# Kernel optimization log

Measured on AMD Instinct MI355X. Metric: run time of the kernel, lower is better.

The kernel has to match this reference:

```python
import jax, jax.numpy as jnp
import numpy as np

VOCAB = 32000
EMBED_DIM = 256
NUM_RULES = 100
BATCH, SEQ = 4, 2048


def setup_inputs() -> dict:
    key = jax.random.key(0)
    k1, k2, k3, k4 = jax.random.split(key, 4)
    token_ids = jax.random.randint(k1, (BATCH, SEQ), 0, VOCAB)
    base_embeddings = jax.random.normal(k2, (VOCAB, EMBED_DIM), dtype=jnp.float32)
    rule_transform = jax.random.normal(k3, (NUM_RULES, EMBED_DIM, EMBED_DIM), dtype=jnp.float32)
    token_rules = jax.random.randint(k4, (VOCAB,), 0, NUM_RULES)
    return {
        "token_ids": token_ids,
        "base_embeddings": base_embeddings,
        "rule_transform": rule_transform,
        "token_rules": token_rules,
    }


def reference(token_ids, base_embeddings, rule_transform, token_rules):
    # base_embeds: [B, S, D]
    base_embeds = base_embeddings[token_ids]
    # per-token rule index: [B, S]
    rule_indices = token_rules[token_ids]
    # per-token (D, D) transform gathered from rule bank: [B, S, D, D]
    rule_matrices = rule_transform[rule_indices]
    # token-routed matvec: out[b,s,e] = sum_d base[b,s,d] * M[b,s,d,e]
    return jnp.einsum('bsd,bsde->bse', base_embeds, rule_matrices)
```

## Files before the change

kernel.cpp:

```cpp
#include <hip/hip_runtime.h>


#define NTOK   8192
#define NRULE  100
#define DIM    256
#define TCH    32
#define NSEG   32
#define SEGCAP 256
#define GSTR   64
#define NCONV  (NRULE * 8)
#define NBLK_A (NCONV + NSEG)

#define BFRAG_U16   (NRULE * 8 * 16 * 64 * 8)
#define WS_SEGCNT   (BFRAG_U16 / 2)
#define WS_SEGLIST  (WS_SEGCNT + NRULE * NSEG)
#define WS_TOTAL_INT (WS_SEGLIST + NRULE * NSEG * SEGCAP)
#define WS_BYTES    ((size_t)WS_TOTAL_INT * 4)

typedef __attribute__((ext_vector_type(8))) short bf16x8;
typedef __attribute__((ext_vector_type(4))) float f32x4;

__device__ __forceinline__ unsigned short f2bf(float f) {
    union { float f; unsigned int u; } c; c.f = f;
    unsigned int u = c.u;
    u = (u + 0x7FFFu + ((u >> 16) & 1u)) >> 16;
    return (unsigned short)u;
}

__global__ __launch_bounds__(256)
void conv_scatter_kernel(const int* __restrict__ token_ids,
                         const int* __restrict__ token_rules,
                         const float* __restrict__ M,
                         int* __restrict__ ws,
                         unsigned short* __restrict__ bf) {
    const int tid = threadIdx.x;
    const int bid = blockIdx.x;

    if (bid >= NCONV) {
        __shared__ int cur[NRULE];
        const int b = bid - NCONV;
        if (tid < NRULE) cur[tid] = 0;
        __syncthreads();
        const int tok = b * SEGCAP + tid;
        const int id  = token_ids[tok];
        const int r   = token_rules[id];
        const int slot = atomicAdd(&cur[r], 1);
        ws[WS_SEGLIST + (r * NSEG + b) * SEGCAP + slot] = tok;
        __syncthreads();
        if (tid < NRULE) ws[WS_SEGCNT + tid * NSEG + b] = cur[tid];
        return;
    }

    __shared__ unsigned short sb[32][DIM];
    const int r  = bid >> 3;
    const int ks = bid & 7;
    const float4* M4 = reinterpret_cast<const float4*>(M) + ((size_t)r * 256 + ks * 32) * 64;
    #pragma unroll
    for (int j = 0; j < 8; ++j) {
        int idx = j * 256 + tid;
        int kl = idx >> 6, c4 = idx & 63;
        float4 v = M4[kl * 64 + c4];
        sb[kl][c4 * 4 + 0] = f2bf(v.x);
        sb[kl][c4 * 4 + 1] = f2bf(v.y);
        sb[kl][c4 * 4 + 2] = f2bf(v.z);
        sb[kl][c4 * 4 + 3] = f2bf(v.w);
    }
    __syncthreads();

    uint4* outp = reinterpret_cast<uint4*>(bf) + ((size_t)(r * 8 + ks) * 16) * 64;
    #pragma unroll
    for (int it = 0; it < 4; ++it) {
        int w = it * 256 + tid;
        int ct = w >> 6, l = w & 63;
        int kb = (l >> 4) * 8, cc = ct * 16 + (l & 15);
        unsigned int d0 = sb[kb + 0][cc] | ((unsigned int)sb[kb + 1][cc] << 16);
        unsigned int d1 = sb[kb + 2][cc] | ((unsigned int)sb[kb + 3][cc] << 16);
        unsigned int d2 = sb[kb + 4][cc] | ((unsigned int)sb[kb + 5][cc] << 16);
        unsigned int d3 = sb[kb + 6][cc] | ((unsigned int)sb[kb + 7][cc] << 16);
        outp[ct * 64 + l] = make_uint4(d0, d1, d2, d3);
    }
}

__global__ __launch_bounds__(512)
void gemm_kernel(const int* __restrict__ token_ids,
                 const float* __restrict__ base_emb,
                 const int* __restrict__ ws,
                 const unsigned short* __restrict__ bfrag,
                 float* __restrict__ out) {
    const int xcd  = blockIdx.x & 7;
    const int base = blockIdx.x >> 3;
    const int tid  = threadIdx.x;
    const int wave = tid >> 6, lane = tid & 63;

    __shared__ unsigned short sa[8 * 2 * 64 * 8];
    __shared__ int sst[TCH];
    __shared__ int s_scnt[13][NSEG];
    __shared__ int s_soff[13][NSEG + 1];
    __shared__ int s_tot[13];
    __shared__ int s_choff[14];

    if (tid < 13 * NSEG) {
        int i = tid >> 5, b = tid & (NSEG - 1);
        int r = xcd + 8 * i;
        s_scnt[i][b] = (r < NRULE) ? ws[WS_SEGCNT + r * NSEG + b] : 0;
    }
    __syncthreads();
    if (tid < 13) {
        int acc = 0;
        #pragma unroll
        for (int b = 0; b < NSEG; ++b) { s_soff[tid][b] = acc; acc += s_scnt[tid][b]; }
        s_soff[tid][NSEG] = acc;
        s_tot[tid] = acc;
    }
    __syncthreads();
    if (tid == 0) {
        int acc = 0; s_choff[0] = 0;
        #pragma unroll
        for (int i = 0; i < 13; ++i) { acc += (s_tot[i] + TCH - 1) / TCH; s_choff[i + 1] = acc; }
    }
    __syncthreads();
    const int total_ch = s_choff[13];

    for (int slot = base; slot < total_ch; slot += GSTR) {
        int i = 0;
        #pragma unroll
        for (int k = 1; k < 13; ++k) if (slot >= s_choff[k]) i = k;
        const int r = xcd + 8 * i;
        const int j = slot - s_choff[i];

        __syncthreads();
        if (tid < TCH) {
            int idx = j * TCH + tid;
            int tok = -1;
            if (idx < s_tot[i]) {
                int lo = 0, hi = NSEG - 1;
                while (lo < hi) {
                    int mid = (lo + hi + 1) >> 1;
                    if (s_soff[i][mid] <= idx) lo = mid; else hi = mid - 1;
                }
                tok = ws[WS_SEGLIST + (r * NSEG + lo) * SEGCAP + (idx - s_soff[i][lo])];
            }
            sst[tid] = tok;
        }
        __syncthreads();

        {
            const int s = tid >> 4, q = tid & 15;
            const int pos = sst[s];
            const int tt = s >> 4, lr = s & 15;
            const float4* row4 = nullptr;
            if (pos >= 0)
                row4 = reinterpret_cast<const float4*>(base_emb + (size_t)token_ids[pos] * DIM);
            #pragma unroll
            for (int jj = 0; jj < 4; ++jj) {
                float4 v = row4 ? row4[q * 4 + jj] : make_float4(0.f, 0.f, 0.f, 0.f);
                const int k0 = q * 16 + jj * 4;
                const int ks = k0 >> 5, koff = k0 & 31;
                const int l = lr | ((koff >> 3) << 4);
                const int e0 = koff & 7;
                ushort4 p;
                p.x = f2bf(v.x); p.y = f2bf(v.y); p.z = f2bf(v.z); p.w = f2bf(v.w);
                *reinterpret_cast<ushort4*>(&sa[((ks * 2 + tt) * 64 + l) * 8 + e0]) = p;
            }
        }
        __syncthreads();

        f32x4 acc[2][2];
        #pragma unroll
        for (int tt = 0; tt < 2; ++tt)
            #pragma unroll
            for (int ctl = 0; ctl < 2; ++ctl)
                acc[tt][ctl] = (f32x4){0.f, 0.f, 0.f, 0.f};

        const bf16x8* Af = reinterpret_cast<const bf16x8*>(sa);
        const bf16x8* Bf = reinterpret_cast<const bf16x8*>(bfrag) + (size_t)r * 8 * 16 * 64;
        const int ct0 = wave * 2;

        #pragma unroll
        for (int ks = 0; ks < 8; ++ks) {
            const bf16x8 a0 = Af[(ks * 2 + 0) * 64 + lane];
            const bf16x8 a1 = Af[(ks * 2 + 1) * 64 + lane];
            const bf16x8 b0 = Bf[(ks * 16 + ct0 + 0) * 64 + lane];
            const bf16x8 b1 = Bf[(ks * 16 + ct0 + 1) * 64 + lane];
            acc[0][0] = __builtin_amdgcn_mfma_f32_16x16x32_bf16(a0, b0, acc[0][0], 0, 0, 0);
            acc[0][1] = __builtin_amdgcn_mfma_f32_16x16x32_bf16(a0, b1, acc[0][1], 0, 0, 0);
            acc[1][0] = __builtin_amdgcn_mfma_f32_16x16x32_bf16(a1, b0, acc[1][0], 0, 0, 0);
            acc[1][1] = __builtin_amdgcn_mfma_f32_16x16x32_bf16(a1, b1, acc[1][1], 0, 0, 0);
        }

        #pragma unroll
        for (int tt = 0; tt < 2; ++tt) {
            #pragma unroll
            for (int reg = 0; reg < 4; ++reg) {
                const int row = tt * 16 + (lane >> 4) * 4 + reg;
                const int pos = sst[row];
                if (pos >= 0) {
                    #pragma unroll
                    for (int ctl = 0; ctl < 2; ++ctl) {
                        const int col = (ct0 + ctl) * 16 + (lane & 15);
                        out[(size_t)pos * DIM + col] = acc[tt][ctl][reg];
                    }
                }
            }
        }
    }
}

__global__ __launch_bounds__(256, 4)
void rule_embed_fallback(const int* __restrict__ token_ids,
                         const float* __restrict__ base_emb,
                         const float* __restrict__ rule_mats,
                         const int* __restrict__ token_rules,
                         float* __restrict__ out, int n_tokens) {
    const int wave = threadIdx.x >> 6, lane = threadIdx.x & 63;
    const int tok = blockIdx.x * 4 + wave;
    __shared__ float base[4][DIM];
    if (tok < n_tokens) {
        const int tid = token_ids[tok];
        reinterpret_cast<float4*>(base[wave])[lane] =
            reinterpret_cast<const float4*>(base_emb + (size_t)tid * DIM)[lane];
    }
    __syncthreads();
    if (tok >= n_tokens) return;
    const int tid = token_ids[tok];
    const int r = token_rules[tid];
    const float4* M4 = reinterpret_cast<const float4*>(rule_mats + (size_t)r * DIM * DIM);
    float4 acc = make_float4(0.f, 0.f, 0.f, 0.f);
    #pragma unroll 8
    for (int d = 0; d < DIM; ++d) {
        const float b = base[wave][d];
        const float4 m = M4[d * (DIM / 4) + lane];
        acc.x += b * m.x; acc.y += b * m.y; acc.z += b * m.z; acc.w += b * m.w;
    }
    reinterpret_cast<float4*>(out + (size_t)tok * DIM)[lane] = acc;
}

extern "C" void kernel_launch(void* const* d_in, const int* in_sizes, int n_in,
                              void* d_out, int out_size, void* d_ws, size_t ws_size,
                              hipStream_t stream) {
    const int*   token_ids   = (const int*)d_in[0];
    const float* base_emb    = (const float*)d_in[1];
    const float* rule_mats   = (const float*)d_in[2];
    const int*   token_rules = (const int*)d_in[3];
    float*       out         = (float*)d_out;

    if (ws_size < WS_BYTES) {
        rule_embed_fallback<<<(NTOK + 3) / 4, 256, 0, stream>>>(
            token_ids, base_emb, rule_mats, token_rules, out, NTOK);
        return;
    }

    int*            ws = (int*)d_ws;
    unsigned short* bf = (unsigned short*)d_ws;

    conv_scatter_kernel<<<NBLK_A, 256, 0, stream>>>(token_ids, token_rules, rule_mats, ws, bf);
    gemm_kernel<<<8 * GSTR, 512, 0, stream>>>(token_ids, base_emb, ws, bf, out);
}
```

Measured before the change: 21.99 us.

## Fuse rule-matrix bf16 conversion into GEMM with double-buffered LDS staging

Drops the separate conversion pass that wrote bf16 MFMA fragments of every rule matrix to workspace. The GEMM kernel now reads fp32 rule-matrix slices directly, converts them to bf16 and stores them in a double-buffered LDS tile per k-step. The grid stride is reduced from 64 to 48. This removes a pre-pass and its workspace round trip, but each 32-token chunk now reloads and reconverts the full 256x256 fp32 matrix (twice the bytes of the bf16 version) and adds a barrier per k-step.

```diff
diff --git a/kernel.cpp b/kernel.cpp
--- a/kernel.cpp
+++ b/kernel.cpp
@@ -7,12 +7,9 @@
 #define TCH    32
 #define NSEG   32
 #define SEGCAP 256
-#define GSTR   64
-#define NCONV  (NRULE * 8)
-#define NBLK_A (NCONV + NSEG)
-
-#define BFRAG_U16   (NRULE * 8 * 16 * 64 * 8)
-#define WS_SEGCNT   (BFRAG_U16 / 2)
+#define GSTR   48
+
+#define WS_SEGCNT   0
 #define WS_SEGLIST  (WS_SEGCNT + NRULE * NSEG)
 #define WS_TOTAL_INT (WS_SEGLIST + NRULE * NSEG * SEGCAP)
 #define WS_BYTES    ((size_t)WS_TOTAL_INT * 4)
@@ -28,64 +25,27 @@
 }
 
 __global__ __launch_bounds__(256)
-void conv_scatter_kernel(const int* __restrict__ token_ids,
-                         const int* __restrict__ token_rules,
-                         const float* __restrict__ M,
-                         int* __restrict__ ws,
-                         unsigned short* __restrict__ bf) {
-    const int tid = threadIdx.x;
-    const int bid = blockIdx.x;
-
-    if (bid >= NCONV) {
-        __shared__ int cur[NRULE];
-        const int b = bid - NCONV;
-        if (tid < NRULE) cur[tid] = 0;
-        __syncthreads();
-        const int tok = b * SEGCAP + tid;
-        const int id  = token_ids[tok];
-        const int r   = token_rules[id];
-        const int slot = atomicAdd(&cur[r], 1);
-        ws[WS_SEGLIST + (r * NSEG + b) * SEGCAP + slot] = tok;
-        __syncthreads();
-        if (tid < NRULE) ws[WS_SEGCNT + tid * NSEG + b] = cur[tid];
-        return;
-    }
-
-    __shared__ unsigned short sb[32][DIM];
-    const int r  = bid >> 3;
-    const int ks = bid & 7;
-    const float4* M4 = reinterpret_cast<const float4*>(M) + ((size_t)r * 256 + ks * 32) * 64;
-    #pragma unroll
-    for (int j = 0; j < 8; ++j) {
-        int idx = j * 256 + tid;
-        int kl = idx >> 6, c4 = idx & 63;
-        float4 v = M4[kl * 64 + c4];
-        sb[kl][c4 * 4 + 0] = f2bf(v.x);
-        sb[kl][c4 * 4 + 1] = f2bf(v.y);
-        sb[kl][c4 * 4 + 2] = f2bf(v.z);
-        sb[kl][c4 * 4 + 3] = f2bf(v.w);
-    }
-    __syncthreads();
-
-    uint4* outp = reinterpret_cast<uint4*>(bf) + ((size_t)(r * 8 + ks) * 16) * 64;
-    #pragma unroll
-    for (int it = 0; it < 4; ++it) {
-        int w = it * 256 + tid;
-        int ct = w >> 6, l = w & 63;
-        int kb = (l >> 4) * 8, cc = ct * 16 + (l & 15);
-        unsigned int d0 = sb[kb + 0][cc] | ((unsigned int)sb[kb + 1][cc] << 16);
-        unsigned int d1 = sb[kb + 2][cc] | ((unsigned int)sb[kb + 3][cc] << 16);
-        unsigned int d2 = sb[kb + 4][cc] | ((unsigned int)sb[kb + 5][cc] << 16);
-        unsigned int d3 = sb[kb + 6][cc] | ((unsigned int)sb[kb + 7][cc] << 16);
-        outp[ct * 64 + l] = make_uint4(d0, d1, d2, d3);
-    }
+void scatter_kernel(const int* __restrict__ token_ids,
+                    const int* __restrict__ token_rules,
+                    int* __restrict__ ws) {
+    __shared__ int cur[NRULE];
+    const int tid = threadIdx.x, b = blockIdx.x;
+    if (tid < NRULE) cur[tid] = 0;
+    __syncthreads();
+    const int tok = b * SEGCAP + tid;
+    const int id  = token_ids[tok];
+    const int r   = token_rules[id];
+    const int slot = atomicAdd(&cur[r], 1);
+    ws[WS_SEGLIST + (r * NSEG + b) * SEGCAP + slot] = tok;
+    __syncthreads();
+    if (tid < NRULE) ws[WS_SEGCNT + tid * NSEG + b] = cur[tid];
 }
 
 __global__ __launch_bounds__(512)
 void gemm_kernel(const int* __restrict__ token_ids,
                  const float* __restrict__ base_emb,
+                 const float* __restrict__ rule_mats,
                  const int* __restrict__ ws,
-                 const unsigned short* __restrict__ bfrag,
                  float* __restrict__ out) {
     const int xcd  = blockIdx.x & 7;
     const int base = blockIdx.x >> 3;
@@ -93,6 +53,7 @@
     const int wave = tid >> 6, lane = tid & 63;
 
     __shared__ unsigned short sa[8 * 2 * 64 * 8];
+    __shared__ unsigned short fb[2][16 * 64 * 8];
     __shared__ int sst[TCH];
     __shared__ int s_scnt[13][NSEG];
     __shared__ int s_soff[13][NSEG + 1];
@@ -120,6 +81,9 @@
     }
     __syncthreads();
     const int total_ch = s_choff[13];
+
+    const int kk = tid >> 4, f4 = tid & 15;
+    const int e  = kk & 7, khi = (kk >> 3) << 4;
 
     for (int slot = base; slot < total_ch; slot += GSTR) {
         int i = 0;
@@ -144,6 +108,8 @@
         }
         __syncthreads();
 
+        const float4* Mr4 = reinterpret_cast<const float4*>(rule_mats + (size_t)r * DIM * DIM);
+
         {
             const int s = tid >> 4, q = tid & 15;
             const int pos = sst[s];
@@ -162,6 +128,19 @@
                 p.x = f2bf(v.x); p.y = f2bf(v.y); p.z = f2bf(v.z); p.w = f2bf(v.w);
                 *reinterpret_cast<ushort4*>(&sa[((ks * 2 + tt) * 64 + l) * 8 + e0]) = p;
             }
+            #pragma unroll
+            for (int jj = 0; jj < 4; ++jj) {
+                const int f4idx = f4 + 16 * jj;
+                const float4 v = Mr4[kk * 64 + f4idx];
+                const int c0 = f4idx * 4;
+                #pragma unroll
+                for (int ii = 0; ii < 4; ++ii) {
+                    const int col = c0 + ii;
+                    const int l = (col & 15) | khi, ct = col >> 4;
+                    const float vv = ii == 0 ? v.x : ii == 1 ? v.y : ii == 2 ? v.z : v.w;
+                    fb[0][((ct * 64 + l) * 8 + e)] = f2bf(vv);
+                }
+            }
         }
         __syncthreads();
 
@@ -173,19 +152,37 @@
                 acc[tt][ctl] = (f32x4){0.f, 0.f, 0.f, 0.f};
 
         const bf16x8* Af = reinterpret_cast<const bf16x8*>(sa);
-        const bf16x8* Bf = reinterpret_cast<const bf16x8*>(bfrag) + (size_t)r * 8 * 16 * 64;
         const int ct0 = wave * 2;
+        int p = 0;
 
         #pragma unroll
         for (int ks = 0; ks < 8; ++ks) {
+            if (ks < 7) {
+                #pragma unroll
+                for (int jj = 0; jj < 4; ++jj) {
+                    const int f4idx = f4 + 16 * jj;
+                    const float4 v = Mr4[((ks + 1) * 32 + kk) * 64 + f4idx];
+                    const int c0 = f4idx * 4;
+                    #pragma unroll
+                    for (int ii = 0; ii < 4; ++ii) {
+                        const int col = c0 + ii;
+                        const int l = (col & 15) | khi, ct = col >> 4;
+                        const float vv = ii == 0 ? v.x : ii == 1 ? v.y : ii == 2 ? v.z : v.w;
+                        fb[p ^ 1][((ct * 64 + l) * 8 + e)] = f2bf(vv);
+                    }
+                }
+            }
+            const bf16x8* Bf = reinterpret_cast<const bf16x8*>(fb[p]);
             const bf16x8 a0 = Af[(ks * 2 + 0) * 64 + lane];
             const bf16x8 a1 = Af[(ks * 2 + 1) * 64 + lane];
-            const bf16x8 b0 = Bf[(ks * 16 + ct0 + 0) * 64 + lane];
-            const bf16x8 b1 = Bf[(ks * 16 + ct0 + 1) * 64 + lane];
+            const bf16x8 b0 = Bf[(ct0 + 0) * 64 + lane];
+            const bf16x8 b1 = Bf[(ct0 + 1) * 64 + lane];
             acc[0][0] = __builtin_amdgcn_mfma_f32_16x16x32_bf16(a0, b0, acc[0][0], 0, 0, 0);
             acc[0][1] = __builtin_amdgcn_mfma_f32_16x16x32_bf16(a0, b1, acc[0][1], 0, 0, 0);
             acc[1][0] = __builtin_amdgcn_mfma_f32_16x16x32_bf16(a1, b0, acc[1][0], 0, 0, 0);
             acc[1][1] = __builtin_amdgcn_mfma_f32_16x16x32_bf16(a1, b1, acc[1][1], 0, 0, 0);
+            __syncthreads();
+            p ^= 1;
         }
 
         #pragma unroll
@@ -250,9 +247,8 @@
         return;
     }
 
-    int*            ws = (int*)d_ws;
-    unsigned short* bf = (unsigned short*)d_ws;
-
-    conv_scatter_kernel<<<NBLK_A, 256, 0, stream>>>(token_ids, token_rules, rule_mats, ws, bf);
-    gemm_kernel<<<8 * GSTR, 512, 0, stream>>>(token_ids, base_emb, ws, bf, out);
-}
+    int* ws = (int*)d_ws;
+
+    scatter_kernel<<<NSEG, 256, 0, stream>>>(token_ids, token_rules, ws);
+    gemm_kernel<<<8 * GSTR, 512, 0, stream>>>(token_ids, base_emb, rule_mats, ws, out);
+}
```

Result: slower. 35.11 us (+59.6%).
